# Kernel optimization log

Measured on AMD Instinct MI355X. Metric: run time of the kernel, lower is better.

Reference implementation:

```python
import jax, jax.numpy as jnp
import numpy as np

D_MODEL = 256
N_HEADS = 8
D_K = D_MODEL // N_HEADS
N = 4096
N_SEG = 16


def setup_inputs() -> dict:
    key = jax.random.key(0)
    ks = jax.random.split(key, 12)
    s = 0.02
    x_q = jax.random.normal(ks[0], (N, D_MODEL), jnp.float32)
    x_kv = jax.random.normal(ks[1], (N, D_MODEL), jnp.float32)
    # same key -> identical segment ids so every query segment exists in kv
    batch = jnp.sort(jax.random.randint(ks[2], (N,), 0, N_SEG)).astype(jnp.int64)
    params = {}
    names = ['Wq', 'Wk', 'Wv', 'Wo']
    for i, n in enumerate(names):
        params[n] = jax.random.normal(ks[3 + i], (D_MODEL, D_MODEL), jnp.float32) * s
        params['b' + n[1]] = jnp.zeros((D_MODEL,), jnp.float32)
    return dict(x_q=x_q, x_kv=x_kv, batch_q=batch, batch_kv=batch, **params)


def reference(x_q, x_kv, batch_q, batch_kv, Wq, bq, Wk, bk, Wv, bv, Wo, bo):
    # projections (torch Linear: x @ W.T + b)
    q = (x_q @ Wq.T + bq).reshape(N, N_HEADS, D_K)   # [Nq, H, dk]
    k = (x_kv @ Wk.T + bk).reshape(N, N_HEADS, D_K)  # [Nkv, H, dk]
    v = (x_kv @ Wv.T + bv).reshape(N, N_HEADS, D_K)
    scores = jnp.einsum('qhd,khd->hqk', q, k) / jnp.sqrt(jnp.float32(D_K))
    mask = batch_q[:, None] == batch_kv[None, :]      # block-diagonal [Nq, Nkv]
    scores = jnp.where(mask[None], scores, -jnp.inf)
    attn = jax.nn.softmax(scores, axis=-1)            # [H, Nq, Nkv]
    out = jnp.einsum('hqk,khd->qhd', attn, v).reshape(N, D_MODEL)
    out = out @ Wo.T + bo
    return out, attn[None]  # match torch's [1, H, Nq, Nkv] attn shape
```

## Files before the change

### kernel.cpp

```cpp
#include <hip/hip_runtime.h>

#define N_TOK 4096
#define DM 256
#define NH 8
#define DK 32
#define QT 16
#define CH 128

using u16 = unsigned short;
using u32 = unsigned int;
using i64 = long long;
typedef float f32x4 __attribute__((ext_vector_type(4)));

__device__ __forceinline__ float bfl(u32 u){ return __uint_as_float(u << 16); }
__device__ __forceinline__ float bfh(u32 u){ return __uint_as_float(u & 0xffff0000u); }
__device__ __forceinline__ u16 f2bf(float f){
    u32 x = __float_as_uint(f);
    x += 0x7fffu + ((x >> 16) & 1u);
    return (u16)(x >> 16);
}

__global__ __launch_bounds__(256)
void bounds_kernel(const void* __restrict__ batch_q, const void* __restrict__ batch_kv,
                   int2* __restrict__ bounds)
{
    int q = blockIdx.x * 256 + threadIdx.x;
    const int* kv32 = (const int*)batch_kv;
    const i64* kv64 = (const i64*)batch_kv;
    bool is64 = (kv32[N_TOK - 1] == 0);
    int s = is64 ? (int)((const i64*)batch_q)[q] : ((const int*)batch_q)[q];
    int lo = 0, hi = N_TOK;
    while (lo < hi){ int m = (lo + hi) >> 1; int v = is64 ? (int)kv64[m] : kv32[m]; if (v < s) lo = m + 1; else hi = m; }
    int lo2 = lo, hi2 = N_TOK;
    while (lo2 < hi2){ int m = (lo2 + hi2) >> 1; int v = is64 ? (int)kv64[m] : kv32[m]; if (v <= s) lo2 = m + 1; else hi2 = m; }
    bounds[q] = make_int2(lo, lo2);
}

template<int OUT_BF16>
__global__ __launch_bounds__(256)
void proj_kernel(const float* __restrict__ x, const float* __restrict__ W,
                 const float* __restrict__ bias, void* __restrict__ outv)
{
    const int ROWS = 16;
    int row0 = blockIdx.x * ROWS;
    int c = threadIdx.x;
    float acc[ROWS];
    float bv = bias[c];
#pragma unroll
    for (int r = 0; r < ROWS; ++r) acc[r] = bv;
    const float4* Wv = (const float4*)(W + (size_t)c * DM);
    for (int i = 0; i < DM / 4; ++i){
        float4 w = Wv[i];
        int d0 = i * 4;
#pragma unroll
        for (int r = 0; r < ROWS; ++r){
            const float* xr = x + (size_t)(row0 + r) * DM + d0;
            acc[r] += xr[0] * w.x + xr[1] * w.y + xr[2] * w.z + xr[3] * w.w;
        }
    }
#pragma unroll
    for (int r = 0; r < ROWS; ++r){
        size_t idx = (size_t)(row0 + r) * DM + c;
        if (OUT_BF16) ((u16*)outv)[idx] = f2bf(acc[r]);
        else          ((float*)outv)[idx] = acc[r];
    }
}

__global__ __launch_bounds__(256)
void proj_kv_kernel(const float* __restrict__ x, const float* __restrict__ Wk,
                    const float* __restrict__ bk, const float* __restrict__ Wv,
                    const float* __restrict__ bv, u16* __restrict__ Kp,
                    u16* __restrict__ Vp)
{
    const int ROWS = 16;
    int row0 = blockIdx.x * ROWS;
    int c = threadIdx.x;
    int hh = c >> 5, dd = c & 31;
    float acck[ROWS], accv[ROWS];
    float bkv = bk[c], bvv = bv[c];
#pragma unroll
    for (int r = 0; r < ROWS; ++r){ acck[r] = bkv; accv[r] = bvv; }
    const float4* Wk4 = (const float4*)(Wk + (size_t)c * DM);
    const float4* Wv4 = (const float4*)(Wv + (size_t)c * DM);
    for (int i = 0; i < DM / 4; ++i){
        float4 wk = Wk4[i];
        float4 wv = Wv4[i];
        int d0 = i * 4;
#pragma unroll
        for (int r = 0; r < ROWS; ++r){
            const float* xr = x + (size_t)(row0 + r) * DM + d0;
            float x0 = xr[0], x1 = xr[1], x2 = xr[2], x3 = xr[3];
            acck[r] += x0 * wk.x + x1 * wk.y + x2 * wk.z + x3 * wk.w;
            accv[r] += x0 * wv.x + x1 * wv.y + x2 * wv.z + x3 * wv.w;
        }
    }
#pragma unroll
    for (int r = 0; r < ROWS; ++r){
        size_t idx = ((size_t)hh * N_TOK + (row0 + r)) * DK + dd;
        Kp[idx] = f2bf(acck[r]);
        Vp[idx] = f2bf(accv[r]);
    }
}

__global__ __launch_bounds__(256)
void zero_kernel(f32x4* __restrict__ p, int n4)
{
    int i = blockIdx.x * 256 + threadIdx.x;
    int stride = gridDim.x * 256;
    f32x4 z = {0.f, 0.f, 0.f, 0.f};
    for (; i < n4; i += stride) __builtin_nontemporal_store(z, &p[i]);
}

__global__ __launch_bounds__(256)
void attn_kernel(const float* __restrict__ Q, const u16* __restrict__ K,
                 const u16* __restrict__ V, const int2* __restrict__ bounds,
                 float* __restrict__ attn, float* __restrict__ O)
{
    __shared__ uint4 kch[CH][5];
    __shared__ uint4 vch[CH][5];

    const int tid = threadIdx.x;
    const int ql  = tid >> 4;
    const int kk  = tid & 15;
    const int h   = blockIdx.y;
    const int q0  = blockIdx.x * QT;
    const int q   = q0 + ql;

    const int2 bq = bounds[q];
    const int lo = bq.x, hi = bq.y;
    const int lo_min = bounds[q0].x;
    const int hi_max = bounds[q0 + QT - 1].y;

    const u16* Kh = K + (size_t)h * N_TOK * DK;
    const u16* Vh = V + (size_t)h * N_TOK * DK;

    float qr[32];
    {
        const float4* qp = (const float4*)(Q + (size_t)q * DM + h * DK);
#pragma unroll
        for (int i = 0; i < 8; ++i){
            float4 t = qp[i];
            qr[4*i+0] = t.x; qr[4*i+1] = t.y; qr[4*i+2] = t.z; qr[4*i+3] = t.w;
        }
    }

    const float scale = 0.17677669529663687f;

    float m = -1e30f, s = 0.f;
    for (int kc = lo_min; kc < hi_max; kc += CH){
        __syncthreads();
        for (int e = tid; e < CH * 4; e += 256){
            int r = e >> 2, p = e & 3;
            if (kc + r < hi_max)
                kch[r][p] = *(const uint4*)(Kh + (size_t)(kc + r) * DK + p * 8);
        }
        __syncthreads();
        int kend = min(CH, hi_max - kc);
        for (int j = kk; j < kend; j += 16){
            int k = kc + j;
            if (k < lo || k >= hi) continue;
            float dot = 0.f;
#pragma unroll
            for (int p = 0; p < 4; ++p){
                uint4 a = kch[j][p];
                dot += qr[8*p+0]*bfl(a.x) + qr[8*p+1]*bfh(a.x);
                dot += qr[8*p+2]*bfl(a.y) + qr[8*p+3]*bfh(a.y);
                dot += qr[8*p+4]*bfl(a.z) + qr[8*p+5]*bfh(a.z);
                dot += qr[8*p+6]*bfl(a.w) + qr[8*p+7]*bfh(a.w);
            }
            float d = dot * scale;
            float mn = fmaxf(m, d);
            s = s * __expf(m - mn) + __expf(d - mn);
            m = mn;
        }
    }
#pragma unroll
    for (int off = 1; off < 16; off <<= 1){
        float mo = __shfl_xor(m, off, 64);
        float so = __shfl_xor(s, off, 64);
        float mn = fmaxf(m, mo);
        s = s * __expf(m - mn) + so * __expf(mo - mn);
        m = mn;
    }
    const float inv = (s > 0.f) ? 1.0f / s : 0.f;

    float o[32];
#pragma unroll
    for (int d = 0; d < 32; ++d) o[d] = 0.f;

    float* arow = attn + ((size_t)h * N_TOK + q) * N_TOK;

    for (int kc = lo_min; kc < hi_max; kc += CH){
        __syncthreads();
        for (int e = tid; e < CH * 4; e += 256){
            int r = e >> 2, p = e & 3;
            if (kc + r < hi_max){
                kch[r][p] = *(const uint4*)(Kh + (size_t)(kc + r) * DK + p * 8);
                vch[r][p] = *(const uint4*)(Vh + (size_t)(kc + r) * DK + p * 8);
            }
        }
        __syncthreads();
        int kend = min(CH, hi_max - kc);
        for (int j = kk; j < kend; j += 16){
            int k = kc + j;
            if (k < lo || k >= hi) continue;
            float dot = 0.f;
#pragma unroll
            for (int p = 0; p < 4; ++p){
                uint4 a = kch[j][p];
                dot += qr[8*p+0]*bfl(a.x) + qr[8*p+1]*bfh(a.x);
                dot += qr[8*p+2]*bfl(a.y) + qr[8*p+3]*bfh(a.y);
                dot += qr[8*p+4]*bfl(a.z) + qr[8*p+5]*bfh(a.z);
                dot += qr[8*p+6]*bfl(a.w) + qr[8*p+7]*bfh(a.w);
            }
            float pr = __expf(dot * scale - m) * inv;
            __builtin_nontemporal_store(pr, &arow[k]);
#pragma unroll
            for (int pp = 0; pp < 4; ++pp){
                uint4 a = vch[j][pp];
                o[8*pp+0] += pr * bfl(a.x); o[8*pp+1] += pr * bfh(a.x);
                o[8*pp+2] += pr * bfl(a.y); o[8*pp+3] += pr * bfh(a.y);
                o[8*pp+4] += pr * bfl(a.z); o[8*pp+5] += pr * bfh(a.z);
                o[8*pp+6] += pr * bfl(a.w); o[8*pp+7] += pr * bfh(a.w);
            }
        }
    }

#pragma unroll
    for (int d = 0; d < 32; ++d){
#pragma unroll
        for (int off = 1; off < 16; off <<= 1)
            o[d] += __shfl_xor(o[d], off, 64);
    }
    float s0 = 0.f, s1 = 0.f;
#pragma unroll
    for (int d = 0; d < 16; ++d)
        if (kk == d){ s0 = o[2*d]; s1 = o[2*d + 1]; }
    *(float2*)(O + (size_t)q * DM + h * DK + 2 * kk) = make_float2(s0, s1);
}

extern "C" void kernel_launch(void* const* d_in, const int* in_sizes, int n_in,
                              void* d_out, int out_size, void* d_ws, size_t ws_size,
                              hipStream_t stream)
{
    const float* x_q  = (const float*)d_in[0];
    const float* x_kv = (const float*)d_in[1];
    const void* batch_q  = d_in[2];
    const void* batch_kv = d_in[3];
    const float* Wq = (const float*)d_in[4];
    const float* bq = (const float*)d_in[5];
    const float* Wk = (const float*)d_in[6];
    const float* bk = (const float*)d_in[7];
    const float* Wv = (const float*)d_in[8];
    const float* bv = (const float*)d_in[9];
    const float* Wo = (const float*)d_in[10];
    const float* bo = (const float*)d_in[11];

    char* ws = (char*)d_ws;
    float* Q  = (float*)ws;
    u16*   Kp = (u16*)(ws + (size_t)4 * 1024 * 1024);
    u16*   Vp = (u16*)(ws + (size_t)6 * 1024 * 1024);
    float* O  = (float*)(ws + (size_t)8 * 1024 * 1024);
    int2* bounds = (int2*)(ws + (size_t)12 * 1024 * 1024);

    float* out  = (float*)d_out;
    float* attn = out + (size_t)N_TOK * DM;

    int n4 = (int)((size_t)NH * N_TOK * N_TOK / 4);
    zero_kernel<<<2048, 256, 0, stream>>>((f32x4*)attn, n4);

    bounds_kernel<<<N_TOK / 256, 256, 0, stream>>>(batch_q, batch_kv, bounds);
    proj_kernel<0><<<N_TOK/16, 256, 0, stream>>>(x_q,  Wq, bq, Q);
    proj_kv_kernel<<<N_TOK/16, 256, 0, stream>>>(x_kv, Wk, bk, Wv, bv, Kp, Vp);
    attn_kernel<<<dim3(N_TOK / QT, NH), 256, 0, stream>>>(Q, Kp, Vp, bounds, attn, O);
    proj_kernel<0><<<N_TOK/16, 256, 0, stream>>>((const float*)O, Wo, bo, out);
}
```

Baseline: 778.3 us.

## Fuse attn zero-fill into attention kernel and shrink projection row tiles

Removes the separate full-matrix zero kernel. Each attention block now writes zeros only to the masked regions of its own rows, outside the segment bounds, so the valid region is no longer written twice. Projection kernels drop from 16 to 8 rows per block to double the grid, and load x as float4. The online-softmax update gets a branch that skips one exp when the max does not change.

Result: faster. 744.7 us (-4.3%).

```diff
diff --git a/kernel.cpp b/kernel.cpp
--- a/kernel.cpp
+++ b/kernel.cpp
@@ -41,7 +41,7 @@
 void proj_kernel(const float* __restrict__ x, const float* __restrict__ W,
                  const float* __restrict__ bias, void* __restrict__ outv)
 {
-    const int ROWS = 16;
+    const int ROWS = 8;
     int row0 = blockIdx.x * ROWS;
     int c = threadIdx.x;
     float acc[ROWS];
@@ -49,13 +49,13 @@
 #pragma unroll
     for (int r = 0; r < ROWS; ++r) acc[r] = bv;
     const float4* Wv = (const float4*)(W + (size_t)c * DM);
+    const float4* xb = (const float4*)(x + (size_t)row0 * DM);
     for (int i = 0; i < DM / 4; ++i){
         float4 w = Wv[i];
-        int d0 = i * 4;
 #pragma unroll
         for (int r = 0; r < ROWS; ++r){
-            const float* xr = x + (size_t)(row0 + r) * DM + d0;
-            acc[r] += xr[0] * w.x + xr[1] * w.y + xr[2] * w.z + xr[3] * w.w;
+            float4 xv = xb[r * (DM / 4) + i];
+            acc[r] += xv.x * w.x + xv.y * w.y + xv.z * w.z + xv.w * w.w;
         }
     }
 #pragma unroll
@@ -72,7 +72,7 @@
                     const float* __restrict__ bv, u16* __restrict__ Kp,
                     u16* __restrict__ Vp)
 {
-    const int ROWS = 16;
+    const int ROWS = 8;
     int row0 = blockIdx.x * ROWS;
     int c = threadIdx.x;
     int hh = c >> 5, dd = c & 31;
@@ -82,16 +82,15 @@
     for (int r = 0; r < ROWS; ++r){ acck[r] = bkv; accv[r] = bvv; }
     const float4* Wk4 = (const float4*)(Wk + (size_t)c * DM);
     const float4* Wv4 = (const float4*)(Wv + (size_t)c * DM);
+    const float4* xb  = (const float4*)(x + (size_t)row0 * DM);
     for (int i = 0; i < DM / 4; ++i){
         float4 wk = Wk4[i];
         float4 wv = Wv4[i];
-        int d0 = i * 4;
 #pragma unroll
         for (int r = 0; r < ROWS; ++r){
-            const float* xr = x + (size_t)(row0 + r) * DM + d0;
-            float x0 = xr[0], x1 = xr[1], x2 = xr[2], x3 = xr[3];
-            acck[r] += x0 * wk.x + x1 * wk.y + x2 * wk.z + x3 * wk.w;
-            accv[r] += x0 * wv.x + x1 * wv.y + x2 * wv.z + x3 * wv.w;
+            float4 xv = xb[r * (DM / 4) + i];
+            acck[r] += xv.x * wk.x + xv.y * wk.y + xv.z * wk.z + xv.w * wk.w;
+            accv[r] += xv.x * wv.x + xv.y * wv.y + xv.z * wv.z + xv.w * wv.w;
         }
     }
 #pragma unroll
@@ -100,15 +99,6 @@
         Kp[idx] = f2bf(acck[r]);
         Vp[idx] = f2bf(accv[r]);
     }
-}
-
-__global__ __launch_bounds__(256)
-void zero_kernel(f32x4* __restrict__ p, int n4)
-{
-    int i = blockIdx.x * 256 + threadIdx.x;
-    int stride = gridDim.x * 256;
-    f32x4 z = {0.f, 0.f, 0.f, 0.f};
-    for (; i < n4; i += stride) __builtin_nontemporal_store(z, &p[i]);
 }
 
 __global__ __launch_bounds__(256)
@@ -169,9 +159,12 @@
                 dot += qr[8*p+6]*bfl(a.w) + qr[8*p+7]*bfh(a.w);
             }
             float d = dot * scale;
-            float mn = fmaxf(m, d);
-            s = s * __expf(m - mn) + __expf(d - mn);
-            m = mn;
+            if (d <= m){
+                s += __expf(d - m);
+            } else {
+                s = s * __expf(m - d) + 1.f;
+                m = d;
+            }
         }
     }
 #pragma unroll
@@ -237,6 +230,23 @@
     for (int d = 0; d < 16; ++d)
         if (kk == d){ s0 = o[2*d]; s1 = o[2*d + 1]; }
     *(float2*)(O + (size_t)q * DM + h * DK + 2 * kk) = make_float2(s0, s1);
+
+    const f32x4 z4 = {0.f, 0.f, 0.f, 0.f};
+    for (int r = 0; r < QT; ++r){
+        int2 br = bounds[q0 + r];
+        float* row = attn + ((size_t)h * N_TOK + (q0 + r)) * N_TOK;
+        f32x4* row4 = (f32x4*)row;
+        int lo4 = br.x >> 2;
+        for (int p = tid; p < lo4; p += 256)
+            __builtin_nontemporal_store(z4, &row4[p]);
+        if (tid < (br.x & 3))
+            __builtin_nontemporal_store(0.f, &row[(lo4 << 2) + tid]);
+        int hb = (br.y + 3) & ~3;
+        if (tid < hb - br.y)
+            __builtin_nontemporal_store(0.f, &row[br.y + tid]);
+        for (int p = (hb >> 2) + tid; p < N_TOK / 4; p += 256)
+            __builtin_nontemporal_store(z4, &row4[p]);
+    }
 }
 
 extern "C" void kernel_launch(void* const* d_in, const int* in_sizes, int n_in,
@@ -266,12 +276,9 @@
     float* out  = (float*)d_out;
     float* attn = out + (size_t)N_TOK * DM;
 
-    int n4 = (int)((size_t)NH * N_TOK * N_TOK / 4);
-    zero_kernel<<<2048, 256, 0, stream>>>((f32x4*)attn, n4);
-
     bounds_kernel<<<N_TOK / 256, 256, 0, stream>>>(batch_q, batch_kv, bounds);
-    proj_kernel<0><<<N_TOK/16, 256, 0, stream>>>(x_q,  Wq, bq, Q);
-    proj_kv_kernel<<<N_TOK/16, 256, 0, stream>>>(x_kv, Wk, bk, Wv, bv, Kp, Vp);
+    proj_kernel<0><<<N_TOK/8, 256, 0, stream>>>(x_q,  Wq, bq, Q);
+    proj_kv_kernel<<<N_TOK/8, 256, 0, stream>>>(x_kv, Wk, bk, Wv, bv, Kp, Vp);
     attn_kernel<<<dim3(N_TOK / QT, NH), 256, 0, stream>>>(Q, Kp, Vp, bounds, attn, O);
-    proj_kernel<0><<<N_TOK/16, 256, 0, stream>>>((const float*)O, Wo, bo, out);
-}
+    proj_kernel<0><<<N_TOK/8, 256, 0, stream>>>((const float*)O, Wo, bo, out);
+}
```
